# Kernel optimization log

Hardware: AMD Instinct MI355X
Metric: run time of the kernel (lower is better)

The kernel has to match this reference:

```python
import jax, jax.numpy as jnp
import numpy as np

K = 7        # kernel_size
G = 16       # group_number
STRIDE = 1
BN_EPS = 1e-5


def setup_inputs() -> dict:
    key = jax.random.key(0)
    ks = jax.random.split(key, 3)
    B, C, H, W = 2, 256, 56, 56
    Cr = C // 4  # reduction_ratio = 4
    x = jax.random.normal(ks[0], (B, C, H, W), dtype=jnp.float32)
    w1 = jax.random.normal(ks[1], (Cr, C), dtype=jnp.float32) * (1.0 / np.sqrt(C))
    b1 = jnp.zeros((Cr,), dtype=jnp.float32)
    gamma = jnp.ones((Cr,), dtype=jnp.float32)
    beta = jnp.zeros((Cr,), dtype=jnp.float32)
    w2 = jax.random.normal(ks[2], (K * K * G, Cr), dtype=jnp.float32) * (1.0 / np.sqrt(Cr))
    b2 = jnp.zeros((K * K * G,), dtype=jnp.float32)
    return {"x": x, "w1": w1, "b1": b1, "gamma": gamma, "beta": beta, "w2": w2, "b2": b2}


def _kernel_gen(x, w1, b1, gamma, beta, w2, b2):
    # 1x1 conv -> BatchNorm (training-mode batch stats) -> ReLU -> 1x1 conv
    t = jnp.einsum('oc,bchw->bohw', w1, x) + b1[None, :, None, None]
    mean = t.mean(axis=(0, 2, 3), keepdims=True)
    var = t.var(axis=(0, 2, 3), keepdims=True)
    t = (t - mean) * jax.lax.rsqrt(var + BN_EPS)
    t = t * gamma[None, :, None, None] + beta[None, :, None, None]
    t = jax.nn.relu(t)
    return jnp.einsum('oc,bchw->bohw', w2, t) + b2[None, :, None, None]


def reference(x, w1, b1, gamma, beta, w2, b2):
    B, C, H, W = x.shape
    nh, nw = H // STRIDE, W // STRIDE  # stride == 1 here
    # kernel generation (stride==1 -> no avg_pool)
    k = _kernel_gen(x, w1, b1, gamma, beta, w2, b2)          # (B, K*K*G, nh, nw)
    kernel = k.reshape(B, K * K, nh, nw, G)                   # raw view, as in torch
    # F.unfold with padding=K//2, stride=1 -> layout (B, C*K*K, L), c-major then k
    p = K // 2
    xp = jnp.pad(x, ((0, 0), (0, 0), (p, p), (p, p)))
    patches = jnp.stack(
        [xp[:, :, i:i + nh, j:j + nw] for i in range(K) for j in range(K)],
        axis=2)                                               # (B, C, K*K, nh, nw)
    flat = patches.reshape(B, C * K * K, nh * nw)             # == torch F.unfold
    ip = flat.reshape(B, C // G, K * K, nh, nw, G)            # raw view, as in torch
    out = (kernel[:, None] * ip).sum(axis=2)                  # (B, C//G, nh, nw, G)
    out = out.reshape(B, C, nh, nw)                           # raw view, as in torch
    return out, kernel
```

## Files before the change

kernel.cpp:

```cpp
#include <hip/hip_runtime.h>

#define HW     3136
#define C_IN   256
#define CR     64
#define KKG    784
#define NB     2
#define NPIX   6272
#define BN_EPS 1e-5f

__device__ float g_P[4 * CR * NPIX];
__device__ float g_T[CR * NPIX];
__device__ float g_stat[2 * CR];
__device__ float g_scale[CR];
__device__ float g_shift[CR];

__global__ __launch_bounds__(256) void k1a_conv1(const float* __restrict__ x,
                                                 const float* __restrict__ w1) {
  if (blockIdx.x == 0 && blockIdx.y == 0 && blockIdx.z == 0 && threadIdx.x < 2 * CR)
    g_stat[threadIdx.x] = 0.0f;

  int p = blockIdx.x * 256 + threadIdx.x;
  if (p >= NPIX) return;
  int o0 = blockIdx.y * 4;
  int kc = blockIdx.z;
  int b  = p / HW;
  int u  = p - b * HW;

  const float* xb = x + ((size_t)(b * C_IN + kc * 64)) * HW + u;
  const float* w  = w1 + kc * 64;

  float a0 = 0.f, a1 = 0.f, a2 = 0.f, a3 = 0.f;
#pragma unroll 8
  for (int c = 0; c < 64; ++c) {
    float xv = xb[(size_t)c * HW];
    a0 += w[(o0 + 0) * C_IN + c] * xv;
    a1 += w[(o0 + 1) * C_IN + c] * xv;
    a2 += w[(o0 + 2) * C_IN + c] * xv;
    a3 += w[(o0 + 3) * C_IN + c] * xv;
  }
  float* pp = g_P + ((size_t)kc * CR + o0) * NPIX + p;
  pp[0 * NPIX] = a0; pp[1 * NPIX] = a1; pp[2 * NPIX] = a2; pp[3 * NPIX] = a3;
}

__global__ __launch_bounds__(256) void k1b_reduce(const float* __restrict__ b1) {
  int p = blockIdx.x * 256 + threadIdx.x;
  int o = blockIdx.y;
  float v = 0.0f;
  bool valid = (p < NPIX);
  if (valid) {
    v = b1[o]
      + g_P[((size_t)0 * CR + o) * NPIX + p]
      + g_P[((size_t)1 * CR + o) * NPIX + p]
      + g_P[((size_t)2 * CR + o) * NPIX + p]
      + g_P[((size_t)3 * CR + o) * NPIX + p];
    g_T[(size_t)o * NPIX + p] = v;
  }
  float s = valid ? v : 0.0f;
  float s2 = s * v * (valid ? 1.0f : 0.0f);
  s2 = valid ? v * v : 0.0f;
#pragma unroll
  for (int off = 32; off > 0; off >>= 1) {
    s  += __shfl_down(s, off);
    s2 += __shfl_down(s2, off);
  }
  __shared__ float sd[8];
  int lane = threadIdx.x & 63, wid = threadIdx.x >> 6;
  if (lane == 0) { sd[wid] = s; sd[4 + wid] = s2; }
  __syncthreads();
  if (threadIdx.x == 0) {
    atomicAdd(&g_stat[o],      sd[0] + sd[1] + sd[2] + sd[3]);
    atomicAdd(&g_stat[CR + o], sd[4] + sd[5] + sd[6] + sd[7]);
  }
}

__global__ void k2_scaleshift(const float* __restrict__ gamma,
                              const float* __restrict__ beta) {
  int o = threadIdx.x;
  float S = g_stat[o], S2 = g_stat[CR + o];
  const float invN = 1.0f / (float)NPIX;
  float mean = S * invN;
  float var  = S2 * invN - mean * mean;
  float inv  = rsqrtf(var + BN_EPS);
  float sc   = gamma[o] * inv;
  g_scale[o] = sc;
  g_shift[o] = beta[o] - mean * sc;
}

__global__ __launch_bounds__(256) void k3_conv2(const float* __restrict__ w2,
                                                const float* __restrict__ b2,
                                                float* __restrict__ kout) {
  int l  = blockIdx.x * 256 + threadIdx.x;
  int o0 = blockIdx.y * 16;
  int b  = blockIdx.z;
  if (l >= HW) return;

  float acc[16];
#pragma unroll
  for (int i = 0; i < 16; ++i) acc[i] = b2[o0 + i];

  const float* Tb = g_T + (size_t)b * HW + l;
  const float* w  = w2 + (size_t)o0 * CR;
#pragma unroll 4
  for (int c = 0; c < CR; ++c) {
    float tv = Tb[(size_t)c * NPIX];
    tv = fmaxf(tv * g_scale[c] + g_shift[c], 0.0f);
#pragma unroll
    for (int i = 0; i < 16; ++i)
      acc[i] += w[i * CR + c] * tv;
  }
  float* kb = kout + (size_t)(b * KKG + o0) * HW + l;
#pragma unroll
  for (int i = 0; i < 16; ++i) kb[(size_t)i * HW] = acc[i];
}

__global__ __launch_bounds__(256) void k4_invol(const float* __restrict__ x,
                                                const float* __restrict__ kout,
                                                float* __restrict__ out) {
  int base = blockIdx.x * 256 + threadIdx.x;
  int b    = blockIdx.y;
  int cg0  = blockIdx.z * 8;

  int s = base / HW;
  int u = base - s * HW;
  int yrow = u / 56;
  int yy0 = yrow - 3;
  int xx0 = (u - yrow * 56) - 3;

  const float* kb = kout + (size_t)b * (KKG * HW) + base;
  const float* xb = x + (size_t)b * (C_IN * HW) + (size_t)cg0 * 50176;

  float acc[8];
#pragma unroll
  for (int i = 0; i < 8; ++i) acc[i] = 0.0f;

#pragma unroll 7
  for (int kk = 0; kk < 49; ++kk) {
    int t16 = 16 * kk + s;
    int d   = t16 / 49;
    int kkp = t16 - d * 49;
    int ki  = kkp / 7;
    int kj  = kkp - ki * 7;
    int yy = yy0 + ki, xx = xx0 + kj;
    float kv = kb[(size_t)kk * 50176];
    int off;
    if ((unsigned)yy < 56u && (unsigned)xx < 56u) {
      off = yy * 56 + xx;
    } else {
      off = 0;
      kv = 0.0f;
    }
    const float* xp = xb + (size_t)d * HW + off;
#pragma unroll
    for (int cg = 0; cg < 8; ++cg)
      acc[cg] += kv * xp[(size_t)cg * 50176];
  }

  float* ob = out + (size_t)b * (C_IN * HW) + (size_t)cg0 * 50176 + base;
#pragma unroll
  for (int cg = 0; cg < 8; ++cg) ob[(size_t)cg * 50176] = acc[cg];
}

extern "C" void kernel_launch(void* const* d_in, const int* in_sizes, int n_in,
                              void* d_out, int out_size, void* d_ws, size_t ws_size,
                              hipStream_t stream) {
  const float* x     = (const float*)d_in[0];
  const float* w1    = (const float*)d_in[1];
  const float* b1    = (const float*)d_in[2];
  const float* gamma = (const float*)d_in[3];
  const float* beta  = (const float*)d_in[4];
  const float* w2    = (const float*)d_in[5];
  const float* b2    = (const float*)d_in[6];

  float* out  = (float*)d_out;
  float* kout = out + (size_t)NB * C_IN * HW;

  k1a_conv1<<<dim3(25, 16, 4), 256, 0, stream>>>(x, w1);
  k1b_reduce<<<dim3(25, CR), 256, 0, stream>>>(b1);
  k2_scaleshift<<<dim3(1), 64, 0, stream>>>(gamma, beta);
  k3_conv2<<<dim3(13, 49, NB), 256, 0, stream>>>(w2, b2, kout);
  k4_invol<<<dim3(196, NB, 2), 256, 0, stream>>>(x, kout, out);
}
```

Baseline: 144.2 us.

## Transpose x into channel-group-interleaved layout and fold BN stats into transpose kernel

```diff
diff --git a/kernel.cpp b/kernel.cpp
--- a/kernel.cpp
+++ b/kernel.cpp
@@ -6,19 +6,17 @@
 #define KKG    784
 #define NB     2
 #define NPIX   6272
+#define NT25   25
 #define BN_EPS 1e-5f
 
 __device__ float g_P[4 * CR * NPIX];
 __device__ float g_T[CR * NPIX];
-__device__ float g_stat[2 * CR];
-__device__ float g_scale[CR];
-__device__ float g_shift[CR];
+__device__ float g_bs[2 * CR * NT25];
+__device__ float g_ss[2 * CR];
+__device__ float g_xg[16 * NPIX * 16];
 
 __global__ __launch_bounds__(256) void k1a_conv1(const float* __restrict__ x,
                                                  const float* __restrict__ w1) {
-  if (blockIdx.x == 0 && blockIdx.y == 0 && blockIdx.z == 0 && threadIdx.x < 2 * CR)
-    g_stat[threadIdx.x] = 0.0f;
-
   int p = blockIdx.x * 256 + threadIdx.x;
   if (p >= NPIX) return;
   int o0 = blockIdx.y * 4;
@@ -45,8 +43,8 @@
 __global__ __launch_bounds__(256) void k1b_reduce(const float* __restrict__ b1) {
   int p = blockIdx.x * 256 + threadIdx.x;
   int o = blockIdx.y;
+  bool valid = (p < NPIX);
   float v = 0.0f;
-  bool valid = (p < NPIX);
   if (valid) {
     v = b1[o]
       + g_P[((size_t)0 * CR + o) * NPIX + p]
@@ -55,9 +53,8 @@
       + g_P[((size_t)3 * CR + o) * NPIX + p];
     g_T[(size_t)o * NPIX + p] = v;
   }
-  float s = valid ? v : 0.0f;
-  float s2 = s * v * (valid ? 1.0f : 0.0f);
-  s2 = valid ? v * v : 0.0f;
+  float s  = valid ? v : 0.0f;
+  float s2 = valid ? v * v : 0.0f;
 #pragma unroll
   for (int off = 32; off > 0; off >>= 1) {
     s  += __shfl_down(s, off);
@@ -68,31 +65,62 @@
   if (lane == 0) { sd[wid] = s; sd[4 + wid] = s2; }
   __syncthreads();
   if (threadIdx.x == 0) {
-    atomicAdd(&g_stat[o],      sd[0] + sd[1] + sd[2] + sd[3]);
-    atomicAdd(&g_stat[CR + o], sd[4] + sd[5] + sd[6] + sd[7]);
-  }
-}
-
-__global__ void k2_scaleshift(const float* __restrict__ gamma,
-                              const float* __restrict__ beta) {
-  int o = threadIdx.x;
-  float S = g_stat[o], S2 = g_stat[CR + o];
-  const float invN = 1.0f / (float)NPIX;
-  float mean = S * invN;
-  float var  = S2 * invN - mean * mean;
-  float inv  = rsqrtf(var + BN_EPS);
-  float sc   = gamma[o] * inv;
-  g_scale[o] = sc;
-  g_shift[o] = beta[o] - mean * sc;
+    g_bs[o * NT25 + blockIdx.x]             = sd[0] + sd[1] + sd[2] + sd[3];
+    g_bs[CR * NT25 + o * NT25 + blockIdx.x] = sd[4] + sd[5] + sd[6] + sd[7];
+  }
+}
+
+__global__ __launch_bounds__(256) void k0t_transpose(const float* __restrict__ x,
+                                                     const float* __restrict__ gamma,
+                                                     const float* __restrict__ beta) {
+  int d = blockIdx.x;
+  int p = blockIdx.y * 256 + threadIdx.x;
+  if (p < NPIX) {
+    int b  = (p >= HW) ? 1 : 0;
+    int hw = p - b * HW;
+    const float* xp = x + ((size_t)(b * C_IN + d)) * HW + hw;
+    float r[16];
+#pragma unroll
+    for (int cg = 0; cg < 16; ++cg)
+      r[cg] = xp[(size_t)cg * (16 * HW)];
+    float4* dst = (float4*)(g_xg + (((size_t)d * NPIX + p) << 4));
+    dst[0] = make_float4(r[0], r[1], r[2], r[3]);
+    dst[1] = make_float4(r[4], r[5], r[6], r[7]);
+    dst[2] = make_float4(r[8], r[9], r[10], r[11]);
+    dst[3] = make_float4(r[12], r[13], r[14], r[15]);
+  }
+  if (blockIdx.x == 0 && blockIdx.y == 0 && threadIdx.x < CR) {
+    int o = threadIdx.x;
+    float S = 0.f, S2 = 0.f;
+#pragma unroll
+    for (int px = 0; px < NT25; ++px) {
+      S  += g_bs[o * NT25 + px];
+      S2 += g_bs[CR * NT25 + o * NT25 + px];
+    }
+    const float invN = 1.0f / (float)NPIX;
+    float mean = S * invN;
+    float var  = S2 * invN - mean * mean;
+    float inv  = rsqrtf(var + BN_EPS);
+    float sc   = gamma[o] * inv;
+    g_ss[o]      = sc;
+    g_ss[CR + o] = beta[o] - mean * sc;
+  }
 }
 
 __global__ __launch_bounds__(256) void k3_conv2(const float* __restrict__ w2,
                                                 const float* __restrict__ b2,
                                                 float* __restrict__ kout) {
+  __shared__ float ssc[CR], ssh[CR];
+  if (threadIdx.x < 2 * CR) {
+    float v = g_ss[threadIdx.x];
+    if (threadIdx.x < CR) ssc[threadIdx.x] = v; else ssh[threadIdx.x - CR] = v;
+  }
+  __syncthreads();
+
   int l  = blockIdx.x * 256 + threadIdx.x;
+  if (l >= HW) return;
   int o0 = blockIdx.y * 16;
   int b  = blockIdx.z;
-  if (l >= HW) return;
 
   float acc[16];
 #pragma unroll
@@ -103,7 +131,7 @@
 #pragma unroll 4
   for (int c = 0; c < CR; ++c) {
     float tv = Tb[(size_t)c * NPIX];
-    tv = fmaxf(tv * g_scale[c] + g_shift[c], 0.0f);
+    tv = fmaxf(tv * ssc[c] + ssh[c], 0.0f);
 #pragma unroll
     for (int i = 0; i < 16; ++i)
       acc[i] += w[i * CR + c] * tv;
@@ -113,8 +141,7 @@
   for (int i = 0; i < 16; ++i) kb[(size_t)i * HW] = acc[i];
 }
 
-__global__ __launch_bounds__(256) void k4_invol(const float* __restrict__ x,
-                                                const float* __restrict__ kout,
+__global__ __launch_bounds__(256) void k4_invol(const float* __restrict__ kout,
                                                 float* __restrict__ out) {
   int base = blockIdx.x * 256 + threadIdx.x;
   int b    = blockIdx.y;
@@ -127,7 +154,6 @@
   int xx0 = (u - yrow * 56) - 3;
 
   const float* kb = kout + (size_t)b * (KKG * HW) + base;
-  const float* xb = x + (size_t)b * (C_IN * HW) + (size_t)cg0 * 50176;
 
   float acc[8];
 #pragma unroll
@@ -149,10 +175,13 @@
       off = 0;
       kv = 0.0f;
     }
-    const float* xp = xb + (size_t)d * HW + off;
-#pragma unroll
-    for (int cg = 0; cg < 8; ++cg)
-      acc[cg] += kv * xp[(size_t)cg * 50176];
+    const float* xp = g_xg + ((((size_t)d * NPIX + b * HW + off) << 4) + cg0);
+    float4 xa = *(const float4*)xp;
+    float4 xb4 = *(const float4*)(xp + 4);
+    acc[0] += kv * xa.x;  acc[1] += kv * xa.y;
+    acc[2] += kv * xa.z;  acc[3] += kv * xa.w;
+    acc[4] += kv * xb4.x; acc[5] += kv * xb4.y;
+    acc[6] += kv * xb4.z; acc[7] += kv * xb4.w;
   }
 
   float* ob = out + (size_t)b * (C_IN * HW) + (size_t)cg0 * 50176 + base;
@@ -176,7 +205,7 @@
 
   k1a_conv1<<<dim3(25, 16, 4), 256, 0, stream>>>(x, w1);
   k1b_reduce<<<dim3(25, CR), 256, 0, stream>>>(b1);
-  k2_scaleshift<<<dim3(1), 64, 0, stream>>>(gamma, beta);
+  k0t_transpose<<<dim3(16, NT25), 256, 0, stream>>>(x, gamma, beta);
   k3_conv2<<<dim3(13, 49, NB), 256, 0, stream>>>(w2, b2, kout);
-  k4_invol<<<dim3(196, NB, 2), 256, 0, stream>>>(x, kout, out);
-}
+  k4_invol<<<dim3(196, NB, 2), 256, 0, stream>>>(kout, out);
+}
```

Result: faster. 141.4 us (-2.0%).
